# Kernel tuning notes

Hardware: AMD Instinct MI355X
Metric: run time of the kernel (lower is better)

Reference implementation:

```python
import jax, jax.numpy as jnp
import numpy as np

B, N, D, H = 32, 512, 768, 12
HD = D // H  # 64
EPS = 1e-5


def layer_norm(x, g, b):
    mu = jnp.mean(x, axis=-1, keepdims=True)
    var = jnp.mean((x - mu) ** 2, axis=-1, keepdims=True)
    return (x - mu) / jnp.sqrt(var + EPS) * g + b


def setup_inputs() -> dict:
    key = jax.random.key(0)
    ks = jax.random.split(key, 10)
    x = jax.random.normal(ks[0], (B, N, D), dtype=jnp.float32)
    adj = jax.random.randint(ks[1], (B, N, N), 0, 2).astype(jnp.int32)
    adj = jnp.maximum(adj, jnp.eye(N, dtype=jnp.int32)[None])  # self-loops
    init = lambda k, shape: (jax.random.normal(k, shape, dtype=jnp.float32) * 0.02)
    return {
        "x": x, "adj": adj,
        "wq": init(ks[2], (D, D)), "bq": jnp.zeros((D,), jnp.float32),
        "wk": init(ks[3], (D, D)), "bk": jnp.zeros((D,), jnp.float32),
        "wv": init(ks[4], (D, D)), "bv": jnp.zeros((D,), jnp.float32),
        "wo": init(ks[5], (D, D)), "bo": jnp.zeros((D,), jnp.float32),
        "g1": jnp.ones((D,), jnp.float32), "b1": jnp.zeros((D,), jnp.float32),
        "g2": jnp.ones((D,), jnp.float32), "b2": jnp.zeros((D,), jnp.float32),
        "w_ffn1": init(ks[6], (D, 4 * D)), "b_ffn1": jnp.zeros((4 * D,), jnp.float32),
        "w_ffn2": init(ks[7], (4 * D, D)), "b_ffn2": jnp.zeros((D,), jnp.float32),
    }


def reference(x, adj, wq, bq, wk, bk, wv, bv, wo, bo, g1, b1, g2, b2,
              w_ffn1, b_ffn1, w_ffn2, b_ffn2):
    scale = HD ** -0.5
    h = layer_norm(x, g1, b1)
    split = lambda t: t.reshape(B, N, H, HD).transpose(0, 2, 1, 3)  # [B,H,N,HD]
    q = split(h @ wq + bq)
    k = split(h @ wk + bk)
    v = split(h @ wv + bv)
    scores = jnp.einsum('bhnd,bhmd->bhnm', q, k) * scale  # [B,H,N,N]
    scores = jnp.where(adj[:, None, :, :] == 0, -jnp.inf, scores)
    attn = jax.nn.softmax(scores, axis=-1)
    attn = jnp.nan_to_num(attn, nan=0.0)  # rows with no edges -> 0
    out = jnp.einsum('bhnm,bhmd->bhnd', attn, v)
    out = out.transpose(0, 2, 1, 3).reshape(B, N, D)
    out = out @ wo + bo + x  # residual (dropout=0, eval mode)
    h2 = layer_norm(out, g2, b2)
    ffn = jax.nn.gelu(h2 @ w_ffn1 + b_ffn1, approximate=False) @ w_ffn2 + b_ffn2
    return out + ffn
```

## Files before the change

kernel.cpp:

```cpp
#include <hip/hip_runtime.h>


#define Bn 32
#define Nn 512
#define Dn 768
#define Hn 12
#define HDn 64
#define Mn (Bn * Nn)
#define DFn 3072
#define MCHUNK 8192

typedef unsigned short u16;
typedef unsigned int u32;
typedef unsigned long long u64;
typedef short bf16x8 __attribute__((ext_vector_type(8)));
typedef float f32x4 __attribute__((ext_vector_type(4)));
typedef unsigned short u16x8 __attribute__((ext_vector_type(8)));
typedef unsigned int u32x2 __attribute__((ext_vector_type(2)));

__device__ __forceinline__ float b2f(u16 u) {
    return __uint_as_float(((unsigned int)u) << 16);
}
__device__ __forceinline__ u16 f2b(float f) {
    unsigned int u = __float_as_uint(f);
    u += 0x7fffu + ((u >> 16) & 1u);
    return (u16)(u >> 16);
}
__device__ __forceinline__ float loadDyn(const void* p, size_t i, int f) {
    return f ? ((const float*)p)[i] : b2f(((const u16*)p)[i]);
}
__device__ __forceinline__ float gelu_exact(float x) {
    return 0.5f * x * (1.0f + erff(x * 0.70710678118654752f));
}

#if __has_builtin(__builtin_amdgcn_exp2f)
#define EXP2F(x) __builtin_amdgcn_exp2f(x)
#else
#define EXP2F(x) __expf((x) * 0.6931471805599453f)
#endif

__device__ __forceinline__ u32 pk_bf16(float lo, float hi) {
    u32 r;
    asm("v_cvt_pk_bf16_f32 %0, %1, %2" : "=v"(r) : "v"(lo), "v"(hi));
    return r;
}

__device__ __forceinline__ void gl_lds16(const u16* g, u16* l) {
    __builtin_amdgcn_global_load_lds(
        (const __attribute__((address_space(1))) void*)(unsigned long long)(const void*)g,
        (__attribute__((address_space(3))) void*)(unsigned)(unsigned long long)(void*)l,
        16, 0, 0);
}

__global__ __launch_bounds__(256) void sniff_k(const u16* __restrict__ x,
                                               int* __restrict__ flag) {
    const int idx = blockIdx.x * 256 + threadIdx.x;
    u16x8 a = *(const u16x8*)&x[(size_t)idx * 8];
    int cnt = 0;
#pragma unroll
    for (int e = 0; e < 8; e++)
        cnt += ((a[e] & 0x7F80) == 0x7F80) ? 1 : 0;
#pragma unroll
    for (int off = 1; off <= 32; off <<= 1) cnt += __shfl_xor(cnt, off, 64);
    if ((threadIdx.x & 63) == 0 && cnt > 0) atomicAdd(flag, cnt);
}

__device__ __forceinline__ int flagval(const int* flagp) {
    return (*flagp > 32) ? 1 : 0;
}

__global__ __launch_bounds__(256) void pack_bias_k(
    const void* __restrict__ bq, const void* __restrict__ bk,
    const void* __restrict__ bv, const void* __restrict__ bo,
    const void* __restrict__ bf1, const void* __restrict__ bf2,
    float* __restrict__ out, const int* __restrict__ flagp) {
    const int f = flagval(flagp);
    const int i = blockIdx.x * 256 + threadIdx.x;
    if (i >= 6912) return;
    const void* src;
    int off;
    if (i < 768)       { src = bq;  off = i; }
    else if (i < 1536) { src = bk;  off = i - 768; }
    else if (i < 2304) { src = bv;  off = i - 1536; }
    else if (i < 3072) { src = bo;  off = i - 2304; }
    else if (i < 6144) { src = bf1; off = i - 3072; }
    else               { src = bf2; off = i - 6144; }
    out[i] = loadDyn(src, off, f);
}

__global__ __launch_bounds__(256) void mask_build_k(
    const int* __restrict__ adj, u64* __restrict__ mask) {
    const int idx = blockIdx.x * 256 + threadIdx.x;
    const size_t base = (size_t)(idx >> 3) * Nn + (size_t)(idx & 7) * 64;
    const int4* p = (const int4*)(adj + base);
    u64 m = 0;
#pragma unroll
    for (int c = 0; c < 16; c++) {
        int4 a = p[c];
        if (a.x) m |= 1ull << (c * 4 + 0);
        if (a.y) m |= 1ull << (c * 4 + 1);
        if (a.z) m |= 1ull << (c * 4 + 2);
        if (a.w) m |= 1ull << (c * 4 + 3);
    }
    mask[idx] = m;
}

__global__ __launch_bounds__(256) void transpose_k(
    const void* __restrict__ in, u16* __restrict__ out, int R, int C,
    const int* __restrict__ flagp) {
    const int f = flagval(flagp);
    __shared__ u16 tile[32][33];
    int c0 = blockIdx.x * 32, r0 = blockIdx.y * 32;
    int tx = threadIdx.x, ty = threadIdx.y;
#pragma unroll
    for (int i = 0; i < 32; i += 8)
        tile[ty + i][tx] = f2b(loadDyn(in, (size_t)(r0 + ty + i) * C + c0 + tx, f));
    __syncthreads();
#pragma unroll
    for (int i = 0; i < 32; i += 8)
        out[(size_t)(c0 + ty + i) * R + r0 + tx] = tile[tx][ty + i];
}

__global__ __launch_bounds__(256) void vtrans_k(
    const u16* __restrict__ v, u16* __restrict__ vt) {
    __shared__ u16 tile[32][33];
    const int bh = blockIdx.z;
    const int d0 = blockIdx.x * 32;
    const int n0 = blockIdx.y * 32;
    const int b = bh / Hn, h = bh % Hn;
    const int tx = threadIdx.x, ty = threadIdx.y;
#pragma unroll
    for (int i = 0; i < 32; i += 8)
        tile[ty + i][tx] =
            v[(size_t)(b * Nn + n0 + ty + i) * Dn + h * HDn + d0 + tx];
    __syncthreads();
#pragma unroll
    for (int i = 0; i < 32; i += 8)
        vt[((size_t)bh * HDn + d0 + ty + i) * Nn + n0 + tx] = tile[tx][ty + i];
}

template <int XDYN>
__global__ __launch_bounds__(256) void ln_k(
    const void* __restrict__ x, const void* __restrict__ g,
    const void* __restrict__ b, u16* __restrict__ y,
    const int* __restrict__ flagp) {
    const int f = flagval(flagp);
    const int t = threadIdx.x;
    const int row = blockIdx.x * 8 + (t >> 5);
    const int l32 = t & 31;
    const size_t base = (size_t)row * Dn;
    float v[24];
    if (XDYN == 0 || f == 0) {
        const u16* xp = (const u16*)x;
#pragma unroll
        for (int kk = 0; kk < 3; kk++) {
            u16x8 a = *(const u16x8*)&xp[base + kk * 256 + l32 * 8];
#pragma unroll
            for (int e = 0; e < 8; e++) v[kk * 8 + e] = b2f(a[e]);
        }
    } else {
#pragma unroll
        for (int kk = 0; kk < 3; kk++)
#pragma unroll
            for (int e = 0; e < 8; e++)
                v[kk * 8 + e] = loadDyn(x, base + kk * 256 + l32 * 8 + e, f);
    }
    float s = 0.f;
#pragma unroll
    for (int i = 0; i < 24; i++) s += v[i];
#pragma unroll
    for (int off = 1; off <= 16; off <<= 1) s += __shfl_xor(s, off, 64);
    const float mu = s * (1.0f / Dn);
    float d2 = 0.f;
#pragma unroll
    for (int i = 0; i < 24; i++) { float d = v[i] - mu; d2 += d * d; }
#pragma unroll
    for (int off = 1; off <= 16; off <<= 1) d2 += __shfl_xor(d2, off, 64);
    const float rstd = rsqrtf(d2 * (1.0f / Dn) + 1e-5f);
#pragma unroll
    for (int kk = 0; kk < 3; kk++) {
        const int c0 = kk * 256 + l32 * 8;
        u16x8 o;
        if (f == 0) {
            u16x8 gv = *(const u16x8*)&((const u16*)g)[c0];
            u16x8 bv = *(const u16x8*)&((const u16*)b)[c0];
#pragma unroll
            for (int e = 0; e < 8; e++)
                o[e] = f2b((v[kk * 8 + e] - mu) * rstd * b2f(gv[e]) + b2f(bv[e]));
        } else {
#pragma unroll
            for (int e = 0; e < 8; e++)
                o[e] = f2b((v[kk * 8 + e] - mu) * rstd * loadDyn(g, c0 + e, f)
                           + loadDyn(b, c0 + e, f));
        }
        *(u16x8*)&y[base + c0] = o;
    }
}

template <int ACT, int RES, int STORE, int BM, int CSPLIT>
__global__ __launch_bounds__(256, (BM == 256 ? 2 : 3)) void gemm_bt(
    const u16* __restrict__ A, const u16* __restrict__ Bt,
    const float* __restrict__ bias, const void* __restrict__ res,
    void* __restrict__ C, int M, int N, int K, int moff, int NY,
    const int* __restrict__ flagp) {
    constexpr int WM = BM / 2;
    constexpr int NI = WM / 16;
    constexpr int NA = BM / 64;
    __shared__ __align__(16) u16 As[3][BM * 32];
    __shared__ __align__(16) u16 Bs[3][128 * 32];
    const int tid = threadIdx.x;

    const int nwg = gridDim.x;
    const int lin = blockIdx.x;
    const int w = (lin & 7) * (nwg >> 3) + (lin >> 3);
    const int mtile = w / NY, ntile = w - mtile * NY;
    const int m0 = mtile * BM, n0 = ntile * 128;

    const int wave = tid >> 6, lane = tid & 63;
    const int wm = (wave & 1) * WM, wn = (wave >> 1) * 64;
    const int lm = lane & 15, quad = lane >> 4;

    const int srow = tid >> 2;
    const int sc = tid & 3;
    const int koff = (sc ^ ((srow >> 1) & 3)) * 8;
    const u16* gA[NA];
    const u16* gB[2];
#pragma unroll
    for (int i = 0; i < NA; i++)
        gA[i] = A + (size_t)(m0 + srow + i * 64) * K + koff;
#pragma unroll
    for (int i = 0; i < 2; i++)
        gB[i] = Bt + (size_t)(n0 + srow + i * 64) * K + koff;

    f32x4 acc[NI][4] = {};

    auto stage = [&](int buf) {
#pragma unroll
        for (int i = 0; i < NA; i++) {
            gl_lds16(gA[i], &As[buf][(tid + i * 256) * 8]);
            gA[i] += 32;
        }
#pragma unroll
        for (int i = 0; i < 2; i++) {
            gl_lds16(gB[i], &Bs[buf][(tid + i * 256) * 8]);
            gB[i] += 32;
        }
    };
    const int rchunk = (quad ^ ((lm >> 1) & 3)) * 8;
    auto compute = [&](int buf) {
        bf16x8 af[NI], bfv[4];
#pragma unroll
        for (int i = 0; i < NI; i++)
            af[i] = *(const bf16x8*)&As[buf][(wm + i * 16 + lm) * 32 + rchunk];
#pragma unroll
        for (int j = 0; j < 4; j++)
            bfv[j] = *(const bf16x8*)&Bs[buf][(wn + j * 16 + lm) * 32 + rchunk];
#pragma unroll
        for (int i = 0; i < NI; i++)
#pragma unroll
            for (int j = 0; j < 4; j++)
                acc[i][j] = __builtin_amdgcn_mfma_f32_16x16x32_bf16(
                    af[i], bfv[j], acc[i][j], 0, 0, 0);
    };

    const int nt = K / 32;
    stage(0);
    stage(1);
    int cur = 0, stg = 2;
    for (int t = 0; t < nt - 1; ++t) {
        if constexpr (BM == 256)
            asm volatile("s_waitcnt vmcnt(6)" ::: "memory");
        else
            asm volatile("s_waitcnt vmcnt(4)" ::: "memory");
        __builtin_amdgcn_s_barrier();
        if (t + 2 < nt) stage(stg);
        compute(cur);
        cur = (cur == 2) ? 0 : cur + 1;
        stg = (stg == 2) ? 0 : stg + 1;
    }
    asm volatile("s_waitcnt vmcnt(0)" ::: "memory");
    __builtin_amdgcn_s_barrier();
    compute(cur);

    const int f = flagval(flagp);
    float bias_f[4];
#pragma unroll
    for (int j = 0; j < 4; j++)
        bias_f[j] = bias[n0 + wn + j * 16 + lm];
#pragma unroll
    for (int i = 0; i < NI; i++) {
#pragma unroll
        for (int r = 0; r < 4; r++) {
            const int row = m0 + wm + i * 16 + quad * 4 + r;
#pragma unroll
            for (int j = 0; j < 4; j++) {
                int col = n0 + wn + j * 16 + lm;
                size_t rb;
                if (CSPLIT > 0) {
                    const int reg = col / CSPLIT;
                    rb = ((size_t)reg * M + moff + row) * (size_t)CSPLIT;
                    col -= reg * CSPLIT;
                } else {
                    rb = (size_t)(moff + row) * N;
                }
                float vv = acc[i][j][r] + bias_f[j];
                if (ACT == 1) vv = gelu_exact(vv);
                if (RES == 1) vv += b2f(((const u16*)res)[rb + col]);
                if (RES == 2) vv += loadDyn(res, rb + col, f);
                if (STORE == 0) ((u16*)C)[rb + col] = f2b(vv);
                else {
                    if (f) ((float*)C)[rb + col] = vv;
                    else   ((u16*)C)[rb + col] = f2b(vv);
                }
            }
        }
    }
}

__global__ __launch_bounds__(256, 4) void attn_mfma_k(
    const u16* q, const u16* __restrict__ k,
    const u16* __restrict__ vt, const u64* __restrict__ mask, u16* o) {
    const int h = blockIdx.x, qg = blockIdx.y, b = blockIdx.z;
    const int q0 = qg * 64;
    const int tid = threadIdx.x;
    const int wave = tid >> 6, lane = tid & 63;
    const int lm = lane & 15, quad = lane >> 4;
    const int wm = wave * 16;
    const int bh = b * Hn + h;
    const float SC2 = 0.125f * 1.4426950408889634f;

    __shared__ __align__(16) u16 Ks[64 * 72];
    __shared__ __align__(16) u16 Vts[64 * 72];
    __shared__ __align__(16) u16 PsT[64 * 72];

    const u16* qrow = q + ((size_t)(b * Nn + q0 + wm + lm)) * Dn + h * HDn + quad * 8;
    const bf16x8 aq0 = *(const bf16x8*)(qrow);
    const bf16x8 aq1 = *(const bf16x8*)(qrow + 32);

    const int srow = tid >> 2, scc = (tid & 3) * 16;
    const u16* kbase = k + ((size_t)(b * Nn + srow)) * Dn + h * HDn + scc;
    const u16* vbase = vt + ((size_t)bh * HDn + srow) * Nn + scc;

    u16x8 kr0 = *(const u16x8*)(kbase);
    u16x8 kr1 = *(const u16x8*)(kbase + 8);
    u16x8 vr0 = *(const u16x8*)(vbase);
    u16x8 vr1 = *(const u16x8*)(vbase + 8);

    float msc = 0.f, l_p = 0.f;
    f32x4 Oacc[4] = {};

    for (int kb = 0; kb < Nn / 64; kb++) {
        __syncthreads();
        *(u16x8*)&Ks[srow * 72 + scc]      = kr0;
        *(u16x8*)&Ks[srow * 72 + scc + 8]  = kr1;
        *(u16x8*)&Vts[srow * 72 + scc]     = vr0;
        *(u16x8*)&Vts[srow * 72 + scc + 8] = vr1;
        __syncthreads();
        if (kb + 1 < Nn / 64) {
            const u16* kn = kbase + (size_t)(kb + 1) * 64 * Dn;
            const u16* vn = vbase + (kb + 1) * 64;
            kr0 = *(const u16x8*)(kn);
            kr1 = *(const u16x8*)(kn + 8);
            vr0 = *(const u16x8*)(vn);
            vr1 = *(const u16x8*)(vn + 8);
        }
        f32x4 sacc[4] = {};
        __builtin_amdgcn_s_setprio(1);
#pragma unroll
        for (int s = 0; s < 2; s++) {
            const bf16x8 aq = s == 0 ? aq0 : aq1;
#pragma unroll
            for (int j = 0; j < 4; j++) {
                bf16x8 ak = *(const bf16x8*)&Ks[(j * 16 + lm) * 72 + s * 32 + quad * 8];
                sacc[j] = __builtin_amdgcn_mfma_f32_16x16x32_bf16(ak, aq, sacc[j], 0, 0, 0);
            }
        }
        __builtin_amdgcn_s_setprio(0);
        const u64 mrow = mask[(size_t)(b * Nn + q0 + wm + lm) * 8 + kb];
        const u32 wlo = ((u32)mrow) >> (quad * 4);
        const u32 whi = ((u32)(mrow >> 32)) >> (quad * 4);
#pragma unroll
        for (int j = 0; j < 4; j++) {
            const u32 w = (j < 2) ? wlo : whi;
            const int sh = (j & 1) * 16;
#pragma unroll
            for (int r = 0; r < 4; r++)
                sacc[j][r] = ((w >> (sh + r)) & 1u) ? sacc[j][r] : -3e38f;
        }
        float mx = fmaxf(fmaxf(sacc[0][0], sacc[0][1]), fmaxf(sacc[0][2], sacc[0][3]));
#pragma unroll
        for (int j = 1; j < 4; j++)
            mx = fmaxf(mx, fmaxf(fmaxf(sacc[j][0], sacc[j][1]),
                                 fmaxf(sacc[j][2], sacc[j][3])));
        mx = fmaxf(mx, __shfl_xor(mx, 16, 64));
        mx = fmaxf(mx, __shfl_xor(mx, 32, 64));
        const float mn = fmaxf(msc, mx * SC2);
        const float alpha = EXP2F(msc - mn);
        msc = mn;
        float sum = 0.f;
#pragma unroll
        for (int j = 0; j < 4; j++)
#pragma unroll
            for (int r = 0; r < 4; r++) {
                const float p = EXP2F(fmaf(sacc[j][r], SC2, -mn));
                sacc[j][r] = p;
                sum += p;
            }
        l_p = l_p * alpha + sum;
#pragma unroll
        for (int j = 0; j < 4; j++)
#pragma unroll
            for (int r = 0; r < 4; r++) Oacc[j][r] *= alpha;
        {
            u16* prow = &PsT[(wm + lm) * 72];
#pragma unroll
            for (int j = 0; j < 4; j++) {
                u32x2 pk;
                pk.x = pk_bf16(sacc[j][0], sacc[j][1]);
                pk.y = pk_bf16(sacc[j][2], sacc[j][3]);
                *(u32x2*)&prow[j * 16 + quad * 4] = pk;
            }
        }
        __builtin_amdgcn_s_setprio(1);
#pragma unroll
        for (int s = 0; s < 2; s++) {
            bf16x8 bp = *(const bf16x8*)&PsT[(wm + lm) * 72 + s * 32 + quad * 8];
#pragma unroll
            for (int j = 0; j < 4; j++) {
                bf16x8 av = *(const bf16x8*)&Vts[(j * 16 + lm) * 72 + s * 32 + quad * 8];
                Oacc[j] = __builtin_amdgcn_mfma_f32_16x16x32_bf16(av, bp, Oacc[j], 0, 0, 0);
            }
        }
        __builtin_amdgcn_s_setprio(0);
    }
    float l = l_p;
    l += __shfl_xor(l, 16, 64);
    l += __shfl_xor(l, 32, 64);
    const float inv = (l > 0.f) ? 1.0f / l : 0.f;
    u16* dst = o + ((size_t)(b * Nn + q0 + wm + lm)) * Dn + h * HDn;
#pragma unroll
    for (int j = 0; j < 4; j++) {
        u32x2 pk;
        pk.x = pk_bf16(Oacc[j][0] * inv, Oacc[j][1] * inv);
        pk.y = pk_bf16(Oacc[j][2] * inv, Oacc[j][3] * inv);
        *(u32x2*)&dst[j * 16 + quad * 4] = pk;
    }
}

extern "C" void kernel_launch(void* const* d_in, const int* in_sizes, int n_in,
                              void* d_out, int out_size, void* d_ws,
                              size_t ws_size, hipStream_t stream) {
    const void* x   = d_in[0];
    const int* adj  = (const int*)d_in[1];
    const void* wq  = d_in[2];
    const void* bq  = d_in[3];
    const void* wk  = d_in[4];
    const void* bk  = d_in[5];
    const void* wv  = d_in[6];
    const void* bv  = d_in[7];
    const void* wo  = d_in[8];
    const void* bo  = d_in[9];
    const void* g1  = d_in[10];
    const void* b1  = d_in[11];
    const void* g2  = d_in[12];
    const void* b2  = d_in[13];
    const void* w1  = d_in[14];
    const void* bf1 = d_in[15];
    const void* w2  = d_in[16];
    const void* bf2 = d_in[17];

    char* ws = (char*)d_ws;
    size_t off = 0;
    auto alloc = [&](size_t bytes) -> char* {
        char* p = ws + off;
        off += (bytes + 255) & ~(size_t)255;
        return p;
    };
    int* flag = (int*)alloc(4);
    u16* wqkvT = (u16*)alloc((size_t)3 * Dn * Dn * 2);
    u16* woT  = (u16*)alloc((size_t)Dn * Dn * 2);
    u16* w1T  = (u16*)alloc((size_t)Dn * DFn * 2);
    u16* w2T  = (u16*)alloc((size_t)Dn * DFn * 2);
    float* biasf = (float*)alloc(6912 * 4);
    u64* maskbuf = (u64*)alloc((size_t)Mn * 8 * 8);
    const size_t S = (size_t)Mn * Dn * 2;
    u16* Rh = (u16*)alloc(S);
    u16* Rq = (u16*)alloc(S);
    u16* Rk = (u16*)alloc(S);
    u16* Rv = (u16*)alloc(S);

    hipMemsetAsync(flag, 0, 4, stream);
    sniff_k<<<64, 256, 0, stream>>>((const u16*)x, flag);
    mask_build_k<<<Mn * 8 / 256, 256, 0, stream>>>(adj, maskbuf);
    pack_bias_k<<<27, 256, 0, stream>>>(bq, bk, bv, bo, bf1, bf2, biasf, flag);

    dim3 tb(32, 8);
    transpose_k<<<dim3(Dn / 32, Dn / 32), tb, 0, stream>>>(wq, wqkvT, Dn, Dn, flag);
    transpose_k<<<dim3(Dn / 32, Dn / 32), tb, 0, stream>>>(wk, wqkvT + (size_t)Dn * Dn, Dn, Dn, flag);
    transpose_k<<<dim3(Dn / 32, Dn / 32), tb, 0, stream>>>(wv, wqkvT + (size_t)2 * Dn * Dn, Dn, Dn, flag);
    transpose_k<<<dim3(Dn / 32, Dn / 32), tb, 0, stream>>>(wo, woT, Dn, Dn, flag);
    transpose_k<<<dim3(DFn / 32, Dn / 32), tb, 0, stream>>>(w1, w1T, Dn, DFn, flag);
    transpose_k<<<dim3(Dn / 32, DFn / 32), tb, 0, stream>>>(w2, w2T, DFn, Dn, flag);

    ln_k<1><<<Mn / 8, 256, 0, stream>>>(x, g1, b1, Rh, flag);

    gemm_bt<0, 0, 0, 256, Dn><<<1152, 256, 0, stream>>>(
        Rh, wqkvT, biasf, nullptr, Rq, Mn, 3 * Dn, Dn, 0, 18, flag);

    vtrans_k<<<dim3(HDn / 32, Nn / 32, Bn * Hn), tb, 0, stream>>>(Rv, Rh);

    attn_mfma_k<<<dim3(Hn, Nn / 64, Bn), 256, 0, stream>>>(Rq, Rk, Rh, maskbuf, Rq);

    gemm_bt<0, 2, 0, 128, 0><<<768, 256, 0, stream>>>(
        Rq, woT, biasf + 2304, x, Rv, Mn, Dn, Dn, 0, 6, flag);

    ln_k<0><<<Mn / 8, 256, 0, stream>>>(Rv, g2, b2, Rh, flag);

    u16* hidden = Rq;
    for (int c = 0; c < Mn / MCHUNK; c++) {
        gemm_bt<1, 0, 0, 256, 0><<<768, 256, 0, stream>>>(
            Rh + (size_t)c * MCHUNK * Dn, w1T, biasf + 3072, nullptr, hidden,
            MCHUNK, DFn, Dn, 0, 24, flag);
        gemm_bt<0, 1, 1, 128, 0><<<384, 256, 0, stream>>>(
            hidden, w2T, biasf + 6144, Rv, d_out, MCHUNK, Dn, DFn, c * MCHUNK, 6, flag);
    }
}
```

Before: 670.3 us.

## Fuse V transpose into QKV GEMM epilogue and use 128-row tiles everywhere

The QKV projection GEMM now writes its V slice directly in the transposed [B,H,HD,N] layout, so the separate vtrans kernel and its extra pass over V are removed. The GEMM template also drops the 256-row tile variant and uses 128x128 tiles with 3 blocks per CU for all GEMMs, doubling grid sizes for QKV and FFN1. Buffer roles are reshuffled to match. The transposed V stores are strided by N, so that part of the epilogue writes scattered 2-byte values. The smaller tiles give less reuse per block.

```diff
diff --git a/kernel.cpp b/kernel.cpp
--- a/kernel.cpp
+++ b/kernel.cpp
@@ -121,24 +121,6 @@
         out[(size_t)(c0 + ty + i) * R + r0 + tx] = tile[tx][ty + i];
 }
 
-__global__ __launch_bounds__(256) void vtrans_k(
-    const u16* __restrict__ v, u16* __restrict__ vt) {
-    __shared__ u16 tile[32][33];
-    const int bh = blockIdx.z;
-    const int d0 = blockIdx.x * 32;
-    const int n0 = blockIdx.y * 32;
-    const int b = bh / Hn, h = bh % Hn;
-    const int tx = threadIdx.x, ty = threadIdx.y;
-#pragma unroll
-    for (int i = 0; i < 32; i += 8)
-        tile[ty + i][tx] =
-            v[(size_t)(b * Nn + n0 + ty + i) * Dn + h * HDn + d0 + tx];
-    __syncthreads();
-#pragma unroll
-    for (int i = 0; i < 32; i += 8)
-        vt[((size_t)bh * HDn + d0 + ty + i) * Nn + n0 + tx] = tile[tx][ty + i];
-}
-
 template <int XDYN>
 __global__ __launch_bounds__(256) void ln_k(
     const void* __restrict__ x, const void* __restrict__ g,
@@ -197,16 +179,13 @@
     }
 }
 
-template <int ACT, int RES, int STORE, int BM, int CSPLIT>
-__global__ __launch_bounds__(256, (BM == 256 ? 2 : 3)) void gemm_bt(
+template <int ACT, int RES, int STORE, int CSPLIT>
+__global__ __launch_bounds__(256, 3) void gemm_bt(
     const u16* __restrict__ A, const u16* __restrict__ Bt,
     const float* __restrict__ bias, const void* __restrict__ res,
     void* __restrict__ C, int M, int N, int K, int moff, int NY,
     const int* __restrict__ flagp) {
-    constexpr int WM = BM / 2;
-    constexpr int NI = WM / 16;
-    constexpr int NA = BM / 64;
-    __shared__ __align__(16) u16 As[3][BM * 32];
+    __shared__ __align__(16) u16 As[3][128 * 32];
     __shared__ __align__(16) u16 Bs[3][128 * 32];
     const int tid = threadIdx.x;
 
@@ -214,29 +193,29 @@
     const int lin = blockIdx.x;
     const int w = (lin & 7) * (nwg >> 3) + (lin >> 3);
     const int mtile = w / NY, ntile = w - mtile * NY;
-    const int m0 = mtile * BM, n0 = ntile * 128;
+    const int m0 = mtile * 128, n0 = ntile * 128;
 
     const int wave = tid >> 6, lane = tid & 63;
-    const int wm = (wave & 1) * WM, wn = (wave >> 1) * 64;
+    const int wm = (wave & 1) * 64, wn = (wave >> 1) * 64;
     const int lm = lane & 15, quad = lane >> 4;
 
     const int srow = tid >> 2;
     const int sc = tid & 3;
     const int koff = (sc ^ ((srow >> 1) & 3)) * 8;
-    const u16* gA[NA];
+    const u16* gA[2];
     const u16* gB[2];
 #pragma unroll
-    for (int i = 0; i < NA; i++)
+    for (int i = 0; i < 2; i++)
         gA[i] = A + (size_t)(m0 + srow + i * 64) * K + koff;
 #pragma unroll
     for (int i = 0; i < 2; i++)
         gB[i] = Bt + (size_t)(n0 + srow + i * 64) * K + koff;
 
-    f32x4 acc[NI][4] = {};
+    f32x4 acc[4][4] = {};
 
     auto stage = [&](int buf) {
 #pragma unroll
-        for (int i = 0; i < NA; i++) {
+        for (int i = 0; i < 2; i++) {
             gl_lds16(gA[i], &As[buf][(tid + i * 256) * 8]);
             gA[i] += 32;
         }
@@ -248,15 +227,15 @@
     };
     const int rchunk = (quad ^ ((lm >> 1) & 3)) * 8;
     auto compute = [&](int buf) {
-        bf16x8 af[NI], bfv[4];
-#pragma unroll
-        for (int i = 0; i < NI; i++)
+        bf16x8 af[4], bfv[4];
+#pragma unroll
+        for (int i = 0; i < 4; i++)
             af[i] = *(const bf16x8*)&As[buf][(wm + i * 16 + lm) * 32 + rchunk];
 #pragma unroll
         for (int j = 0; j < 4; j++)
             bfv[j] = *(const bf16x8*)&Bs[buf][(wn + j * 16 + lm) * 32 + rchunk];
 #pragma unroll
-        for (int i = 0; i < NI; i++)
+        for (int i = 0; i < 4; i++)
 #pragma unroll
             for (int j = 0; j < 4; j++)
                 acc[i][j] = __builtin_amdgcn_mfma_f32_16x16x32_bf16(
@@ -268,10 +247,7 @@
     stage(1);
     int cur = 0, stg = 2;
     for (int t = 0; t < nt - 1; ++t) {
-        if constexpr (BM == 256)
-            asm volatile("s_waitcnt vmcnt(6)" ::: "memory");
-        else
-            asm volatile("s_waitcnt vmcnt(4)" ::: "memory");
+        asm volatile("s_waitcnt vmcnt(4)" ::: "memory");
         __builtin_amdgcn_s_barrier();
         if (t + 2 < nt) stage(stg);
         compute(cur);
@@ -287,30 +263,38 @@
 #pragma unroll
     for (int j = 0; j < 4; j++)
         bias_f[j] = bias[n0 + wn + j * 16 + lm];
-#pragma unroll
-    for (int i = 0; i < NI; i++) {
+    const int reg = (CSPLIT > 0) ? (n0 / CSPLIT) : 0;
+    const int nc0 = n0 - reg * CSPLIT;
+#pragma unroll
+    for (int i = 0; i < 4; i++) {
 #pragma unroll
         for (int r = 0; r < 4; r++) {
             const int row = m0 + wm + i * 16 + quad * 4 + r;
 #pragma unroll
             for (int j = 0; j < 4; j++) {
-                int col = n0 + wn + j * 16 + lm;
-                size_t rb;
-                if (CSPLIT > 0) {
-                    const int reg = col / CSPLIT;
-                    rb = ((size_t)reg * M + moff + row) * (size_t)CSPLIT;
-                    col -= reg * CSPLIT;
-                } else {
-                    rb = (size_t)(moff + row) * N;
-                }
                 float vv = acc[i][j][r] + bias_f[j];
                 if (ACT == 1) vv = gelu_exact(vv);
-                if (RES == 1) vv += b2f(((const u16*)res)[rb + col]);
-                if (RES == 2) vv += loadDyn(res, rb + col, f);
-                if (STORE == 0) ((u16*)C)[rb + col] = f2b(vv);
-                else {
-                    if (f) ((float*)C)[rb + col] = vv;
-                    else   ((u16*)C)[rb + col] = f2b(vv);
+                if (CSPLIT > 0) {
+                    const int lcol = nc0 + wn + j * 16 + lm;
+                    if (reg == 2) {
+                        const int hh = lcol >> 6, dd = lcol & 63;
+                        const int bb = row >> 9, nn = row & (Nn - 1);
+                        ((u16*)C)[(size_t)2 * M * CSPLIT +
+                                  ((size_t)(bb * Hn + hh) * HDn + dd) * Nn + nn] = f2b(vv);
+                    } else {
+                        ((u16*)C)[(size_t)reg * M * CSPLIT +
+                                  (size_t)row * CSPLIT + lcol] = f2b(vv);
+                    }
+                } else {
+                    const int col = n0 + wn + j * 16 + lm;
+                    const size_t rb = (size_t)(moff + row) * N;
+                    if (RES == 1) vv += b2f(((const u16*)res)[rb + col]);
+                    if (RES == 2) vv += loadDyn(res, rb + col, f);
+                    if (STORE == 0) ((u16*)C)[rb + col] = f2b(vv);
+                    else {
+                        if (f) ((float*)C)[rb + col] = vv;
+                        else   ((u16*)C)[rb + col] = f2b(vv);
+                    }
                 }
             }
         }
@@ -504,24 +488,23 @@
 
     ln_k<1><<<Mn / 8, 256, 0, stream>>>(x, g1, b1, Rh, flag);
 
-    gemm_bt<0, 0, 0, 256, Dn><<<1152, 256, 0, stream>>>(
+    gemm_bt<0, 0, 0, Dn><<<2304, 256, 0, stream>>>(
         Rh, wqkvT, biasf, nullptr, Rq, Mn, 3 * Dn, Dn, 0, 18, flag);
 
-    vtrans_k<<<dim3(HDn / 32, Nn / 32, Bn * Hn), tb, 0, stream>>>(Rv, Rh);
-
-    attn_mfma_k<<<dim3(Hn, Nn / 64, Bn), 256, 0, stream>>>(Rq, Rk, Rh, maskbuf, Rq);
-
-    gemm_bt<0, 2, 0, 128, 0><<<768, 256, 0, stream>>>(
-        Rq, woT, biasf + 2304, x, Rv, Mn, Dn, Dn, 0, 6, flag);
-
-    ln_k<0><<<Mn / 8, 256, 0, stream>>>(Rv, g2, b2, Rh, flag);
+    attn_mfma_k<<<dim3(Hn, Nn / 64, Bn), 256, 0, stream>>>(Rq, Rk, Rv, maskbuf, Rq);
+
+    gemm_bt<0, 2, 0, 0><<<768, 256, 0, stream>>>(
+        Rq, woT, biasf + 2304, x, Rh, Mn, Dn, Dn, 0, 6, flag);
+
+    ln_k<0><<<Mn / 8, 256, 0, stream>>>(Rh, g2, b2, Rv, flag);
 
     u16* hidden = Rq;
     for (int c = 0; c < Mn / MCHUNK; c++) {
-        gemm_bt<1, 0, 0, 256, 0><<<768, 256, 0, stream>>>(
-            Rh + (size_t)c * MCHUNK * Dn, w1T, biasf + 3072, nullptr, hidden,
+        gemm_bt<1, 0, 0, 0><<<1536, 256, 0, stream>>>(
+            Rv + (size_t)c * MCHUNK * Dn, w1T, biasf + 3072, nullptr, hidden,
             MCHUNK, DFn, Dn, 0, 24, flag);
-        gemm_bt<0, 1, 1, 128, 0><<<384, 256, 0, stream>>>(
-            hidden, w2T, biasf + 6144, Rv, d_out, MCHUNK, Dn, DFn, c * MCHUNK, 6, flag);
-    }
-}
+        gemm_bt<0, 1, 1, 0><<<384, 256, 0, stream>>>(
+            hidden, w2T, biasf + 6144, Rh, d_out,
+            MCHUNK, Dn, DFn, c * MCHUNK, 6, flag);
+    }
+}
```

Measured after the change: 667.8 us. No clear change (-0.4%).
